# Kernel tuning notes

Measured on AMD Instinct MI355X. Metric: run time of the kernel, lower is better.

## Reference

```python
import jax, jax.numpy as jnp
import numpy as np

N = 50000          # neuron_count
NNZ = 1_600_000    # edges (avg degree 32)
B = 32             # batch
L = 3              # CONNECTOME_LAYER_NUMBER


def setup_inputs() -> dict:
    key = jax.random.key(0)
    k1, k2, k3, k4, k5 = jax.random.split(key, 5)
    x = jax.random.normal(k1, (B, N), dtype=jnp.float32)
    adj_vals = jax.random.uniform(k2, (NNZ,), dtype=jnp.float32)
    w_vals = jax.random.uniform(k3, (NNZ,), dtype=jnp.float32)
    bias = jnp.ones((N,), dtype=jnp.float32)
    row = jax.random.randint(k4, (NNZ,), 0, N, dtype=jnp.int32)
    col = jax.random.randint(k5, (NNZ,), 0, N, dtype=jnp.int32)
    return {"x": x, "adj_vals": adj_vals, "w_vals": w_vals, "bias": bias,
            "row": row, "col": col}


def _spmm(vals, row, col, dense, n):
    # (sparse NxN) @ dense [N, B] via gather + segment_sum scatter
    contrib = vals[:, None] * dense[col]          # [nnz, B]
    return jax.ops.segment_sum(contrib, row, num_segments=n)


def reference(x, adj_vals, w_vals, bias, row, col):
    # Original per layer: x = ((A @ W) @ x^T)^T + bias.
    # We use associativity: (A @ W) @ x^T == A @ (W @ x^T), avoiding the
    # explicit SpGEMM while computing the same linear map.
    n = bias.shape[0]
    xt = x.T                                      # [N, B]
    for _ in range(L):
        wx = _spmm(w_vals, row, col, xt, n)       # W @ x^T -> [N, B]
        xt = _spmm(adj_vals, row, col, wx, n)     # A @ (W @ x^T)
        xt = xt + bias[:, None]                   # broadcast bias over batch
    return xt.T                                   # [B, N]
```

## Files before the change

kernel.cpp:

```cpp
#include <hip/hip_runtime.h>


#define NN 50000
#define NNZ_E 1600000
#define NB (NN * 32)
#define CHUNK 3072
#define NBLK1 ((NNZ_E + CHUNK - 1) / CHUNK)
#define NBIN ((NN + 127) / 128)
#define NH (NBIN * NBLK1)
#define CAP2 5120
#define BCAP 6144
#define LENP (NBIN * BCAP)
#define SCAN_NBLK ((NH + 255) / 256)
#define TIN_BLKS 98

__device__ __forceinline__ int clampi(int v, int hi) {
    v = v < 0 ? 0 : v;
    return v > hi ? hi : v;
}

__device__ __forceinline__ unsigned short f2h(float v) {
    union { _Float16 h; unsigned short u; } cv;
    cv.h = (_Float16)v;
    return cv.u;
}

__device__ __forceinline__ float kv_val(unsigned kv) {
    union { unsigned short u; _Float16 h; } cv;
    cv.u = (unsigned short)(kv >> 16);
    return (float)cv.h;
}

__global__ __launch_bounds__(256) void hist_kernel(const int* __restrict__ row,
                                                   int* __restrict__ hist1,
                                                   const float* __restrict__ x,
                                                   _Float16* __restrict__ xt) {
    __shared__ int h[NBIN];
    int blk = blockIdx.x, tid = threadIdx.x;
    if (blk >= NBLK1) {
        for (int i = (blk - NBLK1) * 256 + tid; i < NB; i += TIN_BLKS * 256) {
            int n = i >> 5;
            int b = i & 31;
            xt[i] = (_Float16)x[b * NN + n];
        }
        return;
    }
    for (int j = tid; j < NBIN; j += 256) h[j] = 0;
    __syncthreads();
    int base = blk * CHUNK;
    int n = NNZ_E - base; if (n > CHUNK) n = CHUNK;
    for (int i = tid; i < n; i += 256)
        atomicAdd(&h[clampi(row[base + i], NN - 1) >> 7], 1);
    __syncthreads();
    for (int j = tid; j < NBIN; j += 256) hist1[j * NBLK1 + blk] = h[j];
}

__global__ void scan_local_kernel(int* __restrict__ data, int n, int* __restrict__ bsum) {
    __shared__ int s[256];
    int i = blockIdx.x * 256 + threadIdx.x;
    int v = (i < n) ? data[i] : 0;
    s[threadIdx.x] = v;
    __syncthreads();
    for (int off = 1; off < 256; off <<= 1) {
        int t = (threadIdx.x >= off) ? s[threadIdx.x - off] : 0;
        __syncthreads();
        s[threadIdx.x] += t;
        __syncthreads();
    }
    if (i < n) data[i] = s[threadIdx.x] - v;
    if (threadIdx.x == 255) bsum[blockIdx.x] = s[threadIdx.x];
}

__global__ __launch_bounds__(256) void scanfin_kernel(int* __restrict__ data, int n,
                                                      const int* __restrict__ bsum, int m,
                                                      int* __restrict__ binstart) {
    __shared__ int sa[1024];
    __shared__ int sb[1024];
    int tid = threadIdx.x;
#pragma unroll
    for (int q = 0; q < 4; ++q) {
        int p = tid + q * 256;
        sa[p] = (p < m) ? bsum[p] : 0;
    }
    __syncthreads();
    int* src = sa;
    int* dst = sb;
    for (int off = 1; off < 1024; off <<= 1) {
#pragma unroll
        for (int q = 0; q < 4; ++q) {
            int p = tid + q * 256;
            int v = src[p];
            if (p >= off) v += src[p - off];
            dst[p] = v;
        }
        __syncthreads();
        int* t = src; src = dst; dst = t;
    }
    int add = (blockIdx.x > 0) ? src[blockIdx.x - 1] : 0;
    int i = blockIdx.x * 256 + tid;
    if (i < n) {
        int v = data[i] + add;
        data[i] = v;
        if (i % NBLK1 == 0) binstart[i / NBLK1] = v;
    }
    if (i == 0) binstart[NBIN] = NNZ_E;
}

__global__ __launch_bounds__(256) void pass1_kernel(
        const int* __restrict__ row, const int* __restrict__ col,
        const float* __restrict__ a, const float* __restrict__ w,
        const int* __restrict__ hist1_off,
        unsigned* __restrict__ k1, unsigned* __restrict__ aw1) {
    __shared__ int h[NBIN];
    __shared__ int hscan[NBIN];
    __shared__ int hoff[NBIN];
    __shared__ int s256[256];
    __shared__ unsigned sKey[CHUNK];
    __shared__ unsigned sAW[CHUNK];
    int blk = blockIdx.x, tid = threadIdx.x;
    int base = blk * CHUNK;
    int n = NNZ_E - base; if (n > CHUNK) n = CHUNK;

    for (int j = tid; j < NBIN; j += 256) {
        h[j] = 0;
        hoff[j] = hist1_off[j * NBLK1 + blk];
    }
    __syncthreads();
    for (int i = tid; i < n; i += 256)
        atomicAdd(&h[clampi(row[base + i], NN - 1) >> 7], 1);
    __syncthreads();
    int j0 = tid * 2, j1 = tid * 2 + 1;
    int c0 = (j0 < NBIN) ? h[j0] : 0;
    int c1 = (j1 < NBIN) ? h[j1] : 0;
    int tsum = c0 + c1;
    s256[tid] = tsum;
    __syncthreads();
    for (int off = 1; off < 256; off <<= 1) {
        int t = (tid >= off) ? s256[tid - off] : 0;
        __syncthreads();
        s256[tid] += t;
        __syncthreads();
    }
    int ex = s256[tid] - tsum;
    __syncthreads();
    if (j0 < NBIN) { hscan[j0] = ex;      h[j0] = ex; }
    if (j1 < NBIN) { hscan[j1] = ex + c0; h[j1] = ex + c0; }
    __syncthreads();
    for (int i = tid; i < n; i += 256) {
        int r = clampi(row[base + i], NN - 1);
        int c = clampi(col[base + i], NN - 1);
        int bin = r >> 7;
        int p = atomicAdd(&h[bin], 1);
        p = clampi(p, n - 1);
        sKey[p] = ((unsigned)r << 16) | (unsigned)c;
        sAW[p] = ((unsigned)f2h(a[base + i]) << 16) | (unsigned)f2h(w[base + i]);
    }
    __syncthreads();
    for (int p = tid; p < n; p += 256) {
        unsigned key = sKey[p];
        int bin = (int)(key >> 23);
        int d = clampi(hoff[bin] + (p - hscan[bin]), NNZ_E - 1);
        k1[d] = key;
        aw1[d] = sAW[p];
    }
}

__global__ __launch_bounds__(256) void pass2_kernel(
        const unsigned* __restrict__ k1, const unsigned* __restrict__ aw1,
        const int* __restrict__ binstart,
        unsigned* __restrict__ kvA2, unsigned* __restrict__ kvW2,
        unsigned* __restrict__ row_desc) {
    __shared__ unsigned sKey[CAP2];
    __shared__ unsigned sAW[CAP2];
    __shared__ int rh[128];
    __shared__ int rs[128];
    __shared__ int cur[128];
    int bin = blockIdx.x, tid = threadIdx.x;
    int r0 = bin << 7;
    int rows = NN - r0; if (rows > 128) rows = 128;
    int base = clampi(binstart[bin], NNZ_E);
    int size = clampi(binstart[bin + 1], NNZ_E) - base;
    size = clampi(size, CAP2);
    int pbase = bin * BCAP;

    if (tid < 128) rh[tid] = 0;
    __syncthreads();
    for (int i = tid; i < size; i += 256) {
        unsigned key = k1[base + i];
        atomicAdd(&rh[(key >> 16) & 127], 1);
        sKey[i] = key;
        sAW[i] = aw1[base + i];
    }
    __syncthreads();
    int cnt  = (tid < 128) ? rh[tid] : 0;
    int plen = (cnt + 7) & ~7;
    if (tid < 128) rs[tid] = plen;
    __syncthreads();
    for (int off = 1; off < 128; off <<= 1) {
        int t = (tid >= off && tid < 128) ? rs[tid - off] : 0;
        __syncthreads();
        if (tid < 128) rs[tid] += t;
        __syncthreads();
    }
    int rofs = (tid < 128) ? clampi(rs[tid] - plen, BCAP - 8) : 0;
    if (tid < 128) cur[tid] = rofs;
    if (tid < rows)
        row_desc[r0 + tid] = (unsigned)(pbase + rofs) | ((unsigned)(plen >> 3) << 24);
    __syncthreads();
    for (int i = tid; i < size; i += 256) {
        unsigned key = sKey[i];
        unsigned aw  = sAW[i];
        int rl = (key >> 16) & 127;
        int p = atomicAdd(&cur[rl], 1);
        p = clampi(p, BCAP - 1);
        unsigned c = key & 0xFFFFu;
        kvA2[pbase + p] = (aw & 0xFFFF0000u) | c;
        kvW2[pbase + p] = (aw << 16) | c;
    }
    __syncthreads();
    if (tid < rows) {
        int pl = (rh[tid] + 7) & ~7;
        for (int q = rh[tid]; q < pl; ++q) {
            int d = clampi(rofs + q, BCAP - 1);
            kvA2[pbase + d] = 0u;
            kvW2[pbase + d] = 0u;
        }
    }
}

template <int WITH_BIAS, int FINAL>
__global__ __launch_bounds__(256) void spmm_kernel(
        const uint2* __restrict__ kv2, const unsigned* __restrict__ row_desc,
        const unsigned* __restrict__ in32, unsigned* __restrict__ out32,
        const float* __restrict__ bias, float outScale, float biasScale,
        float* __restrict__ outf) {
    int t = blockIdx.x * 256 + threadIdx.x;
    int r = t >> 4;
    int l = t & 15;
    if (r >= NN) return;
    unsigned d = row_desc[r];
    int niter = (int)(d >> 24);
    int base2 = clampi((int)(d & 0xFFFFFFu), LENP - 8) >> 1;
    float accL = 0.0f, accH = 0.0f;
    uint2 k2[4];
    if (niter > 0) {
#pragma unroll
        for (int q = 0; q < 4; ++q) k2[q] = kv2[base2 + q];
    }
    for (int it = 0; it < niter; ++it) {
        unsigned k[8];
#pragma unroll
        for (int q = 0; q < 4; ++q) { k[2 * q] = k2[q].x; k[2 * q + 1] = k2[q].y; }
        unsigned gd[8];
#pragma unroll
        for (int j = 0; j < 8; ++j) gd[j] = in32[((k[j] & 0xFFFFu) << 4) + l];
        if (it + 1 < niter) {
            int nb2 = base2 + (it + 1) * 4;
#pragma unroll
            for (int q = 0; q < 4; ++q) k2[q] = kv2[nb2 + q];
        }
#pragma unroll
        for (int j = 0; j < 8; ++j) {
            float v = kv_val(k[j]);
            union { unsigned u; _Float16 h[2]; } cv;
            cv.u = gd[j];
            accL += v * (float)cv.h[0];
            accH += v * (float)cv.h[1];
        }
    }
    float rL = accL * outScale, rH = accH * outScale;
    if (WITH_BIAS) {
        float bb = bias[r] * biasScale;
        rL += bb; rH += bb;
    }
    if (FINAL) {
        outf[(2 * l) * NN + r]     = rL * 16777216.0f;
        outf[(2 * l + 1) * NN + r] = rH * 16777216.0f;
    } else {
        union { unsigned u; _Float16 h[2]; } o;
        o.h[0] = (_Float16)rL;
        o.h[1] = (_Float16)rH;
        out32[(r << 4) + l] = o.u;
    }
}

extern "C" void kernel_launch(void* const* d_in, const int* in_sizes, int n_in,
                              void* d_out, int out_size, void* d_ws, size_t ws_size,
                              hipStream_t stream) {
    const float* x        = (const float*)d_in[0];
    const float* adj_vals = (const float*)d_in[1];
    const float* w_vals   = (const float*)d_in[2];
    const float* bias     = (const float*)d_in[3];
    const int*   row      = (const int*)d_in[4];
    const int*   col      = (const int*)d_in[5];
    float* out = (float*)d_out;

    unsigned*  k1        = (unsigned*)d_ws;
    unsigned*  aw1       = k1 + NNZ_E;
    unsigned*  kvA2      = aw1 + NNZ_E;
    unsigned*  kvW2      = kvA2 + LENP;
    _Float16*  xt16      = (_Float16*)(kvW2 + LENP);
    _Float16*  tmp16     = xt16 + NB;
    int*   hist1         = (int*)(tmp16 + NB);
    int*   bsumB         = hist1 + NH;
    int*   binstart      = bsumB + 1024;
    unsigned* row_desc   = (unsigned*)(binstart + NBIN + 8);

    const int BS = 256;
    const int grid_spmm = (NN * 16 + BS - 1) / BS;

    hist_kernel<<<NBLK1 + TIN_BLKS, BS, 0, stream>>>(row, hist1, x, xt16);
    scan_local_kernel<<<SCAN_NBLK, BS, 0, stream>>>(hist1, NH, bsumB);
    scanfin_kernel<<<SCAN_NBLK, BS, 0, stream>>>(hist1, NH, bsumB, SCAN_NBLK, binstart);

    pass1_kernel<<<NBLK1, BS, 0, stream>>>(row, col, adj_vals, w_vals,
                                           hist1, k1, aw1);
    pass2_kernel<<<NBIN, BS, 0, stream>>>(k1, aw1, binstart, kvA2, kvW2, row_desc);

    const uint2* kvA = (const uint2*)kvA2;
    const uint2* kvW = (const uint2*)kvW2;
    const unsigned* xt32  = (const unsigned*)xt16;
    unsigned*       xt32w = (unsigned*)xt16;
    const unsigned* tm32  = (const unsigned*)tmp16;
    unsigned*       tm32w = (unsigned*)tmp16;

    const float r256 = 1.0f / 256.0f;
    spmm_kernel<0, 0><<<grid_spmm, BS, 0, stream>>>(kvW, row_desc, xt32, tm32w,
                                                    nullptr, 1.0f, 0.0f, nullptr);
    spmm_kernel<1, 0><<<grid_spmm, BS, 0, stream>>>(kvA, row_desc, tm32, xt32w,
                                                    bias, r256, 1.0f / 256.0f, nullptr);
    spmm_kernel<0, 0><<<grid_spmm, BS, 0, stream>>>(kvW, row_desc, xt32, tm32w,
                                                    nullptr, 1.0f, 0.0f, nullptr);
    spmm_kernel<1, 0><<<grid_spmm, BS, 0, stream>>>(kvA, row_desc, tm32, xt32w,
                                                    bias, r256, 1.0f / 65536.0f, nullptr);
    spmm_kernel<0, 0><<<grid_spmm, BS, 0, stream>>>(kvW, row_desc, xt32, tm32w,
                                                    nullptr, 1.0f, 0.0f, nullptr);
    spmm_kernel<1, 1><<<grid_spmm, BS, 0, stream>>>(kvA, row_desc, tm32, xt32w,
                                                    bias, r256, 1.0f / 16777216.0f, out);
}
```

Before: 241.2 us.

## Use 64-row bins and decouple histogram and scatter chunk sizes

Halves the row-bin width from 128 to 64, which doubles the bin count to 782 and shrinks pass2's per-bin shared buffers. The histogram now uses larger 6144-edge chunks, while pass1 uses smaller 1536-edge chunks, four per histogram chunk. Each pass1 block claims its output offsets with global atomicAdd on the shared histogram prefix. This is meant to raise parallelism and occupancy in pass1 and pass2 and to shrink the scan. The cost is global atomics, and the order of edges inside a bin is no longer deterministic.

```diff
diff --git a/kernel.cpp b/kernel.cpp
--- a/kernel.cpp
+++ b/kernel.cpp
@@ -4,12 +4,14 @@
 #define NN 50000
 #define NNZ_E 1600000
 #define NB (NN * 32)
-#define CHUNK 3072
-#define NBLK1 ((NNZ_E + CHUNK - 1) / CHUNK)
-#define NBIN ((NN + 127) / 128)
-#define NH (NBIN * NBLK1)
-#define CAP2 5120
-#define BCAP 6144
+#define CHUNK_H 6144
+#define NBLK_H ((NNZ_E + CHUNK_H - 1) / CHUNK_H)
+#define CHUNK1 1536
+#define NBLK1P ((NNZ_E + CHUNK1 - 1) / CHUNK1)
+#define NBIN ((NN + 63) / 64)
+#define NH (NBIN * NBLK_H)
+#define CAP2 2816
+#define BCAP 3328
 #define LENP (NBIN * BCAP)
 #define SCAN_NBLK ((NH + 255) / 256)
 #define TIN_BLKS 98
@@ -37,8 +39,8 @@
                                                    _Float16* __restrict__ xt) {
     __shared__ int h[NBIN];
     int blk = blockIdx.x, tid = threadIdx.x;
-    if (blk >= NBLK1) {
-        for (int i = (blk - NBLK1) * 256 + tid; i < NB; i += TIN_BLKS * 256) {
+    if (blk >= NBLK_H) {
+        for (int i = (blk - NBLK_H) * 256 + tid; i < NB; i += TIN_BLKS * 256) {
             int n = i >> 5;
             int b = i & 31;
             xt[i] = (_Float16)x[b * NN + n];
@@ -47,12 +49,12 @@
     }
     for (int j = tid; j < NBIN; j += 256) h[j] = 0;
     __syncthreads();
-    int base = blk * CHUNK;
-    int n = NNZ_E - base; if (n > CHUNK) n = CHUNK;
+    int base = blk * CHUNK_H;
+    int n = NNZ_E - base; if (n > CHUNK_H) n = CHUNK_H;
     for (int i = tid; i < n; i += 256)
-        atomicAdd(&h[clampi(row[base + i], NN - 1) >> 7], 1);
-    __syncthreads();
-    for (int j = tid; j < NBIN; j += 256) hist1[j * NBLK1 + blk] = h[j];
+        atomicAdd(&h[clampi(row[base + i], NN - 1) >> 6], 1);
+    __syncthreads();
+    for (int j = tid; j < NBIN; j += 256) hist1[j * NBLK_H + blk] = h[j];
 }
 
 __global__ void scan_local_kernel(int* __restrict__ data, int n, int* __restrict__ bsum) {
@@ -101,7 +103,7 @@
     if (i < n) {
         int v = data[i] + add;
         data[i] = v;
-        if (i % NBLK1 == 0) binstart[i / NBLK1] = v;
+        if (i % NBLK_H == 0) binstart[i / NBLK_H] = v;
     }
     if (i == 0) binstart[NBIN] = NNZ_E;
 }
@@ -109,30 +111,32 @@
 __global__ __launch_bounds__(256) void pass1_kernel(
         const int* __restrict__ row, const int* __restrict__ col,
         const float* __restrict__ a, const float* __restrict__ w,
-        const int* __restrict__ hist1_off,
+        int* __restrict__ hist1_cur,
         unsigned* __restrict__ k1, unsigned* __restrict__ aw1) {
     __shared__ int h[NBIN];
     __shared__ int hscan[NBIN];
     __shared__ int hoff[NBIN];
     __shared__ int s256[256];
-    __shared__ unsigned sKey[CHUNK];
-    __shared__ unsigned sAW[CHUNK];
+    __shared__ unsigned sKey[CHUNK1];
+    __shared__ unsigned sAW[CHUNK1];
     int blk = blockIdx.x, tid = threadIdx.x;
-    int base = blk * CHUNK;
-    int n = NNZ_E - base; if (n > CHUNK) n = CHUNK;
-
-    for (int j = tid; j < NBIN; j += 256) {
-        h[j] = 0;
-        hoff[j] = hist1_off[j * NBLK1 + blk];
-    }
+    int hblk = blk >> 2;
+    int base = blk * CHUNK1;
+    int n = NNZ_E - base; if (n > CHUNK1) n = CHUNK1;
+
+    for (int j = tid; j < NBIN; j += 256) h[j] = 0;
     __syncthreads();
     for (int i = tid; i < n; i += 256)
-        atomicAdd(&h[clampi(row[base + i], NN - 1) >> 7], 1);
-    __syncthreads();
-    int j0 = tid * 2, j1 = tid * 2 + 1;
-    int c0 = (j0 < NBIN) ? h[j0] : 0;
-    int c1 = (j1 < NBIN) ? h[j1] : 0;
-    int tsum = c0 + c1;
+        atomicAdd(&h[clampi(row[base + i], NN - 1) >> 6], 1);
+    __syncthreads();
+    int c[4];
+    int tsum = 0;
+#pragma unroll
+    for (int q = 0; q < 4; ++q) {
+        int j = tid * 4 + q;
+        c[q] = (j < NBIN) ? h[j] : 0;
+        tsum += c[q];
+    }
     s256[tid] = tsum;
     __syncthreads();
     for (int off = 1; off < 256; off <<= 1) {
@@ -143,22 +147,31 @@
     }
     int ex = s256[tid] - tsum;
     __syncthreads();
-    if (j0 < NBIN) { hscan[j0] = ex;      h[j0] = ex; }
-    if (j1 < NBIN) { hscan[j1] = ex + c0; h[j1] = ex + c0; }
+    int run = ex;
+#pragma unroll
+    for (int q = 0; q < 4; ++q) {
+        int j = tid * 4 + q;
+        if (j < NBIN) {
+            hscan[j] = run;
+            h[j] = run;
+            hoff[j] = c[q] ? atomicAdd(&hist1_cur[j * NBLK_H + hblk], c[q]) : 0;
+            run += c[q];
+        }
+    }
     __syncthreads();
     for (int i = tid; i < n; i += 256) {
         int r = clampi(row[base + i], NN - 1);
-        int c = clampi(col[base + i], NN - 1);
-        int bin = r >> 7;
+        int cc = clampi(col[base + i], NN - 1);
+        int bin = r >> 6;
         int p = atomicAdd(&h[bin], 1);
         p = clampi(p, n - 1);
-        sKey[p] = ((unsigned)r << 16) | (unsigned)c;
+        sKey[p] = ((unsigned)r << 16) | (unsigned)cc;
         sAW[p] = ((unsigned)f2h(a[base + i]) << 16) | (unsigned)f2h(w[base + i]);
     }
     __syncthreads();
     for (int p = tid; p < n; p += 256) {
         unsigned key = sKey[p];
-        int bin = (int)(key >> 23);
+        int bin = (int)(key >> 22);
         int d = clampi(hoff[bin] + (p - hscan[bin]), NNZ_E - 1);
         k1[d] = key;
         aw1[d] = sAW[p];
@@ -172,50 +185,50 @@
         unsigned* __restrict__ row_desc) {
     __shared__ unsigned sKey[CAP2];
     __shared__ unsigned sAW[CAP2];
-    __shared__ int rh[128];
-    __shared__ int rs[128];
-    __shared__ int cur[128];
+    __shared__ int rh[64];
+    __shared__ int rs[64];
+    __shared__ int cur[64];
     int bin = blockIdx.x, tid = threadIdx.x;
-    int r0 = bin << 7;
-    int rows = NN - r0; if (rows > 128) rows = 128;
+    int r0 = bin << 6;
+    int rows = NN - r0; if (rows > 64) rows = 64;
     int base = clampi(binstart[bin], NNZ_E);
     int size = clampi(binstart[bin + 1], NNZ_E) - base;
     size = clampi(size, CAP2);
     int pbase = bin * BCAP;
 
-    if (tid < 128) rh[tid] = 0;
+    if (tid < 64) rh[tid] = 0;
     __syncthreads();
     for (int i = tid; i < size; i += 256) {
         unsigned key = k1[base + i];
-        atomicAdd(&rh[(key >> 16) & 127], 1);
+        atomicAdd(&rh[(key >> 16) & 63], 1);
         sKey[i] = key;
         sAW[i] = aw1[base + i];
     }
     __syncthreads();
-    int cnt  = (tid < 128) ? rh[tid] : 0;
+    int cnt  = (tid < 64) ? rh[tid] : 0;
     int plen = (cnt + 7) & ~7;
-    if (tid < 128) rs[tid] = plen;
-    __syncthreads();
-    for (int off = 1; off < 128; off <<= 1) {
-        int t = (tid >= off && tid < 128) ? rs[tid - off] : 0;
-        __syncthreads();
-        if (tid < 128) rs[tid] += t;
-        __syncthreads();
-    }
-    int rofs = (tid < 128) ? clampi(rs[tid] - plen, BCAP - 8) : 0;
-    if (tid < 128) cur[tid] = rofs;
+    if (tid < 64) rs[tid] = plen;
+    __syncthreads();
+    for (int off = 1; off < 64; off <<= 1) {
+        int t = (tid >= off && tid < 64) ? rs[tid - off] : 0;
+        __syncthreads();
+        if (tid < 64) rs[tid] += t;
+        __syncthreads();
+    }
+    int rofs = (tid < 64) ? clampi(rs[tid] - plen, BCAP - 8) : 0;
+    if (tid < 64) cur[tid] = rofs;
     if (tid < rows)
         row_desc[r0 + tid] = (unsigned)(pbase + rofs) | ((unsigned)(plen >> 3) << 24);
     __syncthreads();
     for (int i = tid; i < size; i += 256) {
         unsigned key = sKey[i];
         unsigned aw  = sAW[i];
-        int rl = (key >> 16) & 127;
+        int rl = (key >> 16) & 63;
         int p = atomicAdd(&cur[rl], 1);
         p = clampi(p, BCAP - 1);
-        unsigned c = key & 0xFFFFu;
-        kvA2[pbase + p] = (aw & 0xFFFF0000u) | c;
-        kvW2[pbase + p] = (aw << 16) | c;
+        unsigned cc = key & 0xFFFFu;
+        kvA2[pbase + p] = (aw & 0xFFFF0000u) | cc;
+        kvW2[pbase + p] = (aw << 16) | cc;
     }
     __syncthreads();
     if (tid < rows) {
@@ -309,12 +322,12 @@
     const int BS = 256;
     const int grid_spmm = (NN * 16 + BS - 1) / BS;
 
-    hist_kernel<<<NBLK1 + TIN_BLKS, BS, 0, stream>>>(row, hist1, x, xt16);
+    hist_kernel<<<NBLK_H + TIN_BLKS, BS, 0, stream>>>(row, hist1, x, xt16);
     scan_local_kernel<<<SCAN_NBLK, BS, 0, stream>>>(hist1, NH, bsumB);
     scanfin_kernel<<<SCAN_NBLK, BS, 0, stream>>>(hist1, NH, bsumB, SCAN_NBLK, binstart);
 
-    pass1_kernel<<<NBLK1, BS, 0, stream>>>(row, col, adj_vals, w_vals,
-                                           hist1, k1, aw1);
+    pass1_kernel<<<NBLK1P, BS, 0, stream>>>(row, col, adj_vals, w_vals,
+                                            hist1, k1, aw1);
     pass2_kernel<<<NBIN, BS, 0, stream>>>(k1, aw1, binstart, kvA2, kvW2, row_desc);
 
     const uint2* kvA = (const uint2*)kvA2;
```

Measured after the change: 283.2 us. 1.17x slower.
